# Kernel tuning notes

Hardware: AMD Instinct MI355X
Metric: run time of the kernel (lower is better)

Reference implementation:

```python
import jax, jax.numpy as jnp
import numpy as np

B, N, C, H = 4, 1024, 1024, 16
HD = C // H
SCALE = HD ** -0.5


def _init_linear(key, out_dim, in_dim):
    # torch nn.Linear default init: U(-1/sqrt(in), 1/sqrt(in)) for weight and bias
    kw, kb = jax.random.split(key)
    bound = 1.0 / np.sqrt(in_dim)
    W = jax.random.uniform(kw, (out_dim, in_dim), jnp.float32, -bound, bound)
    b = jax.random.uniform(kb, (out_dim,), jnp.float32, -bound, bound)
    return W, b


def setup_inputs() -> dict:
    key = jax.random.key(0)
    ks = jax.random.split(key, 5)
    x = jax.random.normal(ks[0], (B, N, C), jnp.float32)
    # NdLinear qkv: Linear(N->N) along seq axis, then Linear(C->3C) along channel axis
    Wq0, bq0 = _init_linear(ks[1], N, N)
    Wq1, bq1 = _init_linear(ks[2], 3 * C, C)
    # NdLinear proj: Linear(N->N) along seq axis, then Linear(C->C) along channel axis
    Wp0, bp0 = _init_linear(ks[3], N, N)
    Wp1, bp1 = _init_linear(ks[4], C, C)
    return {"x": x, "Wq0": Wq0, "bq0": bq0, "Wq1": Wq1, "bq1": bq1,
            "Wp0": Wp0, "bp0": bp0, "Wp1": Wp1, "bp1": bp1}


def _ndlinear(x, W0, b0, W1, b1):
    # NdLinear over (seq, channel): apply Linear along axis 1, then axis 2.
    # torch Linear: y = x @ W.T + b
    x = jnp.einsum('bnc,mn->bmc', x, W0) + b0[None, :, None]   # seq axis
    x = jnp.einsum('bnc,dc->bnd', x, W1) + b1                  # channel axis
    return x


def reference(x, Wq0, bq0, Wq1, bq1, Wp0, bp0, Wp1, bp1):
    qkv = _ndlinear(x, Wq0, bq0, Wq1, bq1)                     # (B, N, 3C)
    qkv = qkv.reshape(B, N, 3, H, HD).transpose(2, 0, 3, 1, 4) # (3, B, H, N, HD)
    q, k, v = qkv[0], qkv[1], qkv[2]
    attn = jnp.einsum('bhnd,bhmd->bhnm', q, k) * SCALE         # (B, H, N, N)
    attn = jax.nn.softmax(attn, axis=-1)
    out = jnp.einsum('bhnm,bhmd->bhnd', attn, v)               # (B, H, N, HD)
    out = out.transpose(0, 2, 1, 3).reshape(B, N, C)
    out = _ndlinear(out, Wp0, bp0, Wp1, bp1)
    return out
```

## Files before the change

### kernel.cpp

```cpp
#include <hip/hip_runtime.h>
#include <hip/hip_bf16.h>
#include <stdint.h>

typedef __bf16 bf16;
typedef __bf16 bf16x4 __attribute__((ext_vector_type(4)));
typedef __bf16 bf16x8 __attribute__((ext_vector_type(8)));
typedef float f32x4 __attribute__((ext_vector_type(4)));

#define B_ 4
#define N_ 1024
#define C_ 1024
#define H_ 16
#define MEG (1u << 20)

__device__ __forceinline__ uint32_t lds_off(const void* p) {
    return (uint32_t)(uintptr_t)p;
}
__device__ __forceinline__ void g2l16(const void* g, uint32_t lds_byte) {
    __builtin_amdgcn_global_load_lds(
        (const __attribute__((address_space(1))) unsigned int*)(uintptr_t)g,
        (__attribute__((address_space(3))) unsigned int*)(uintptr_t)lds_byte,
        16, 0, 0);
}

__global__ __launch_bounds__(256) void cvt4_k(
    const float* __restrict__ s0, bf16* __restrict__ d0,
    const float* __restrict__ s1, bf16* __restrict__ d1,
    const float* __restrict__ s2, bf16* __restrict__ d2,
    const float* __restrict__ s3, bf16* __restrict__ d3) {
    int bid = blockIdx.x;
    const float* s; bf16* d; int base;
    if (bid < 512)       { s = s0; d = d0; base = 0; }
    else if (bid < 2048) { s = s1; d = d1; base = 512; }
    else if (bid < 2560) { s = s2; d = d2; base = 2048; }
    else                 { s = s3; d = d3; base = 2560; }
    int i = ((bid - base) * 256 + threadIdx.x) * 8;
    float4 a = *(const float4*)(s + i);
    float4 b = *(const float4*)(s + i + 4);
    bf16x8 r;
    r[0] = (bf16)a.x; r[1] = (bf16)a.y; r[2] = (bf16)a.z; r[3] = (bf16)a.w;
    r[4] = (bf16)b.x; r[5] = (bf16)b.y; r[6] = (bf16)b.z; r[7] = (bf16)b.w;
    *(bf16x8*)(d + i) = r;
}

__global__ __launch_bounds__(256) void xpose_k(const float* __restrict__ x,
                                               bf16* __restrict__ xT) {
    __shared__ bf16 t[64][66];
    const int tid = threadIdx.x;
    const int b = blockIdx.z, n0 = blockIdx.y * 64, c0 = blockIdx.x * 64;
    {
        int nl = tid >> 2, seg = tid & 3;
        const float* src = x + ((size_t)b * N_ + n0 + nl) * C_ + c0 + seg * 16;
#pragma unroll
        for (int i = 0; i < 4; ++i) {
            float4 v = *(const float4*)(src + i * 4);
            t[nl][seg * 16 + i * 4 + 0] = (bf16)v.x;
            t[nl][seg * 16 + i * 4 + 1] = (bf16)v.y;
            t[nl][seg * 16 + i * 4 + 2] = (bf16)v.z;
            t[nl][seg * 16 + i * 4 + 3] = (bf16)v.w;
        }
    }
    __syncthreads();
    {
        int cl = tid >> 2, seg = tid & 3;
        bf16* dst = xT + ((size_t)b * C_ + c0 + cl) * N_ + n0 + seg * 16;
        bf16x8 o0, o1;
#pragma unroll
        for (int j = 0; j < 8; ++j) o0[j] = t[seg * 16 + j][cl];
#pragma unroll
        for (int j = 0; j < 8; ++j) o1[j] = t[seg * 16 + 8 + j][cl];
        *(bf16x8*)dst = o0;
        *(bf16x8*)(dst + 8) = o1;
    }
}

template <int BIAS, bool OF32>
__global__ __launch_bounds__(512) void gemm_k(
    const bf16* __restrict__ A, const bf16* __restrict__ Bm,
    const float* __restrict__ bias, void* __restrict__ Cv,
    int M, int Nn, int K, long long sA, long long sB, long long sC)
{
    __shared__ bf16 smem[2][2][128 * 64];

    const int tid = threadIdx.x;
    const int lane = tid & 63, wid = tid >> 6;
    const int lr = lane & 15, lg = lane >> 4;
    const int wr = wid >> 2, wc = wid & 3;
    const int m0 = blockIdx.y * 128, n0 = blockIdx.x * 128;

    const bf16* Ab = A + (size_t)blockIdx.z * sA;
    const bf16* Bb = Bm + (size_t)blockIdx.z * sB;

    const uint32_t a_lds0 = lds_off(&smem[0][0][0]);
    const uint32_t b_lds0 = lds_off(&smem[0][1][0]);
    const uint32_t bufstride = 2 * 128 * 64 * 2;

    auto stage = [&](int kt, int buf) {
#pragma unroll
        for (int half = 0; half < 2; ++half) {
            int it = tid + half * 512;
            int r = it >> 3, ch = it & 7;
            int sch = ch ^ (r & 7);
            g2l16(Ab + (size_t)(m0 + r) * K + kt * 64 + sch * 8,
                  a_lds0 + buf * bufstride + it * 16);
            g2l16(Bb + (size_t)(n0 + r) * K + kt * 64 + sch * 8,
                  b_lds0 + buf * bufstride + it * 16);
        }
    };

    f32x4 acc[4][2];
#pragma unroll
    for (int i = 0; i < 4; ++i)
#pragma unroll
        for (int j = 0; j < 2; ++j) { f32x4 z = {0.f,0.f,0.f,0.f}; acc[i][j] = z; }

    stage(0, 0);
    __syncthreads();

    const int nt = K >> 6;
    for (int t = 0; t < nt; ++t) {
        int buf = t & 1;
        if (t + 1 < nt) stage(t + 1, buf ^ 1);
        const bf16* As = &smem[buf][0][0];
        const bf16* Bs = &smem[buf][1][0];
#pragma unroll
        for (int s = 0; s < 2; ++s) {
            bf16x8 af[4], bfr[2];
#pragma unroll
            for (int mi = 0; mi < 4; ++mi) {
                int row = wr * 64 + mi * 16 + lr;
                int slot = (s * 4 + lg) ^ (row & 7);
                af[mi] = *(const bf16x8*)(As + row * 64 + slot * 8);
            }
#pragma unroll
            for (int ni = 0; ni < 2; ++ni) {
                int row = wc * 32 + ni * 16 + lr;
                int slot = (s * 4 + lg) ^ (row & 7);
                bfr[ni] = *(const bf16x8*)(Bs + row * 64 + slot * 8);
            }
#pragma unroll
            for (int mi = 0; mi < 4; ++mi)
#pragma unroll
                for (int ni = 0; ni < 2; ++ni)
                    acc[mi][ni] = __builtin_amdgcn_mfma_f32_16x16x32_bf16(
                        af[mi], bfr[ni], acc[mi][ni], 0, 0, 0);
        }
        __syncthreads();
    }

#pragma unroll
    for (int mi = 0; mi < 4; ++mi)
#pragma unroll
        for (int ni = 0; ni < 2; ++ni)
#pragma unroll
            for (int r = 0; r < 4; ++r) {
                int row = m0 + wr * 64 + mi * 16 + lg * 4 + r;
                int col = n0 + wc * 32 + ni * 16 + lr;
                float bv = (BIAS == 0) ? bias[row] : bias[col];
                float v = acc[mi][ni][r] + bv;
                if constexpr (OF32)
                    ((float*)Cv + (size_t)blockIdx.z * sC)[(size_t)row * Nn + col] = v;
                else
                    ((bf16*)Cv + (size_t)blockIdx.z * sC)[(size_t)row * Nn + col] = (bf16)v;
            }
}

__global__ __launch_bounds__(512) void attn_k(
    const bf16* __restrict__ qkv, bf16* __restrict__ aoT)
{
    __shared__ bf16 Ks[2][4096];
    __shared__ bf16 Vs[2][4096];
    __shared__ bf16 pbuf[8][1024];

    const int tid = threadIdx.x;
    const int lane = tid & 63, wid = tid >> 6;
    const int lr = lane & 15, lg = lane >> 4;
    const int bid = blockIdx.x;
    const int qt = bid >> 6, hb = bid & 63;
    const int b = hb >> 4, h = hb & 15;
    const int qrow0 = qt * 128 + wid * 16;
    const int hoff = h * 64;
    const bf16* qkvb = qkv + (size_t)b * (N_ * 3 * C_);

    bf16x8 qf[2];
#pragma unroll
    for (int kk = 0; kk < 2; ++kk) {
        qf[kk] = *(const bf16x8*)(qkvb + (size_t)(qrow0 + lr) * 3072 +
                                  hoff + kk * 32 + lg * 8);
#pragma unroll
        for (int j = 0; j < 8; ++j)
            qf[kk][j] = (bf16)((float)qf[kk][j] * 0.18033688f);
    }

    const uint32_t ks0 = lds_off(&Ks[0][0]);
    const int vd = tid & 63, vkg = tid >> 6;

    auto stageK = [&](int kt, int buf) {
        int key = tid >> 3, ch = tid & 7;
        int sch = ch ^ (key & 7);
        g2l16(qkvb + (size_t)(kt * 64 + key) * 3072 + C_ + hoff + sch * 8,
              ks0 + buf * 8192 + tid * 16);
    };
    auto loadV = [&](int kt) -> bf16x8 {
        const bf16* base = qkvb + 2 * C_ + hoff + vd;
        bf16x8 v;
#pragma unroll
        for (int j = 0; j < 8; ++j)
            v[j] = base[(size_t)(kt * 64 + vkg * 8 + j) * 3072];
        return v;
    };
    auto writeV = [&](bf16x8 v, int buf) {
        *(bf16x8*)(&Vs[buf][vd * 64 + ((vkg ^ (vd & 7)) * 8)]) = v;
    };

    float lsum = 0.f;
    f32x4 o[4];
#pragma unroll
    for (int i = 0; i < 4; ++i) { f32x4 z = {0.f,0.f,0.f,0.f}; o[i] = z; }

    char* prow = (char*)&pbuf[wid][0] + lr * 128;
    const int swz = (lr & 7) << 4;

    stageK(0, 0);
    writeV(loadV(0), 0);
    __syncthreads();

    for (int kt = 0; kt < 16; ++kt) {
        int buf = kt & 1;
        bf16x8 vnext;
        if (kt + 1 < 16) {
            stageK(kt + 1, buf ^ 1);
            vnext = loadV(kt + 1);
        }

        f32x4 s[4];
        __builtin_amdgcn_s_setprio(1);
#pragma unroll
        for (int st = 0; st < 4; ++st) {
            f32x4 z = {0.f, 0.f, 0.f, 0.f};
#pragma unroll
            for (int kk = 0; kk < 2; ++kk) {
                int row = st * 16 + lr;
                int slot = (kk * 4 + lg) ^ (row & 7);
                bf16x8 kf = *(const bf16x8*)(&Ks[buf][row * 64 + slot * 8]);
                z = __builtin_amdgcn_mfma_f32_16x16x32_bf16(kf, qf[kk], z, 0, 0, 0);
            }
            s[st] = z;
        }
        __builtin_amdgcn_s_setprio(0);

#pragma unroll
        for (int st = 0; st < 4; ++st) {
            bf16x4 w;
#pragma unroll
            for (int r = 0; r < 4; ++r) {
                float e = __builtin_amdgcn_exp2f(s[st][r]);
                w[r] = (bf16)e;
                lsum += e;
            }
            *(bf16x4*)(prow + ((st * 32 + lg * 8) ^ swz)) = w;
        }

        bf16x8 pf[2];
        pf[0] = *(const bf16x8*)(prow + ((lg * 16) ^ swz));
        pf[1] = *(const bf16x8*)(prow + ((64 + lg * 16) ^ swz));

        __builtin_amdgcn_s_setprio(1);
#pragma unroll
        for (int dt = 0; dt < 4; ++dt) {
            int row = dt * 16 + lr;
            bf16x8 v0 = *(const bf16x8*)(&Vs[buf][row * 64 + ((lg ^ (lr & 7)) * 8)]);
            bf16x8 v1 = *(const bf16x8*)(&Vs[buf][row * 64 + (((4 + lg) ^ (lr & 7)) * 8)]);
            o[dt] = __builtin_amdgcn_mfma_f32_16x16x32_bf16(pf[0], v0, o[dt], 0, 0, 0);
            o[dt] = __builtin_amdgcn_mfma_f32_16x16x32_bf16(pf[1], v1, o[dt], 0, 0, 0);
        }
        __builtin_amdgcn_s_setprio(0);

        if (kt + 1 < 16) writeV(vnext, buf ^ 1);
        __syncthreads();
    }

    lsum += __shfl_xor(lsum, 16, 64);
    lsum += __shfl_xor(lsum, 32, 64);
    float rtot = 1.0f / lsum;
    float rcpo[4];
#pragma unroll
    for (int r = 0; r < 4; ++r) rcpo[r] = __shfl(rtot, lg * 4 + r, 64);

#pragma unroll
    for (int dt = 0; dt < 4; ++dt) {
        bf16x4 ov;
#pragma unroll
        for (int r = 0; r < 4; ++r) ov[r] = (bf16)(o[dt][r] * rcpo[r]);
        size_t c = (size_t)b * C_ + hoff + dt * 16 + lr;
        *(bf16x4*)(aoT + c * N_ + qrow0 + lg * 4) = ov;
    }
}

extern "C" void kernel_launch(void* const* d_in, const int* in_sizes, int n_in,
                              void* d_out, int out_size, void* d_ws, size_t ws_size,
                              hipStream_t stream) {
    (void)in_sizes; (void)n_in; (void)out_size; (void)ws_size;
    const float* x   = (const float*)d_in[0];
    const float* Wq0 = (const float*)d_in[1];
    const float* bq0 = (const float*)d_in[2];
    const float* Wq1 = (const float*)d_in[3];
    const float* bq1 = (const float*)d_in[4];
    const float* Wp0 = (const float*)d_in[5];
    const float* bp0 = (const float*)d_in[6];
    const float* Wp1 = (const float*)d_in[7];
    const float* bp1 = (const float*)d_in[8];

    bf16* ws   = (bf16*)d_ws;
    bf16* xT   = ws;
    bf16* Wq0b = ws + 4 * MEG;
    bf16* Wq1b = ws + 5 * MEG;
    bf16* Wp0b = ws + 8 * MEG;
    bf16* Wp1b = ws + 9 * MEG;
    bf16* y1   = ws + 10 * MEG;
    bf16* y2   = ws + 14 * MEG;
    bf16* aoT  = y1;
    bf16* z1   = y2;
    float* outp = (float*)d_out;

    const long long s1M = (long long)N_ * C_;

    cvt4_k<<<dim3(3072), 256, 0, stream>>>(Wq0, Wq0b, Wq1, Wq1b,
                                           Wp0, Wp0b, Wp1, Wp1b);
    xpose_k<<<dim3(16, 16, 4), 256, 0, stream>>>(x, xT);

    gemm_k<0, false><<<dim3(8, 8, 4), 512, 0, stream>>>(
        Wq0b, xT, bq0, y1, 1024, 1024, 1024, 0LL, s1M, s1M);
    gemm_k<1, false><<<dim3(24, 32, 1), 512, 0, stream>>>(
        y1, Wq1b, bq1, y2, 4096, 3072, 1024, 0LL, 0LL, 0LL);
    attn_k<<<dim3(512), 512, 0, stream>>>(y2, aoT);
    gemm_k<0, false><<<dim3(8, 8, 4), 512, 0, stream>>>(
        Wp0b, aoT, bp0, z1, 1024, 1024, 1024, 0LL, s1M, s1M);
    gemm_k<1, true><<<dim3(8, 32, 1), 512, 0, stream>>>(
        z1, Wp1b, bp1, outp, 4096, 1024, 1024, 0LL, 0LL, 0LL);
}
```

Before: 121.1 us.

## Merge weight-convert and transpose kernels; split attention into 64-row query tiles

Folds the fp32-to-bf16 weight conversion and the x transpose into a single prep launch, saving one kernel launch. The attention kernel now uses 256 threads with 64 query rows per block and 1024 blocks instead of 512, to spread the work over more CUs on the MI355X. Each thread now stages two K chunks and two V chunks per tile, so K/V global traffic per query row doubles in exchange for more parallelism.

Measured after the change: 123.1 us. No clear change (+1.6%).

```diff
diff --git a/kernel.cpp b/kernel.cpp
--- a/kernel.cpp
+++ b/kernel.cpp
@@ -23,31 +23,33 @@
         16, 0, 0);
 }
 
-__global__ __launch_bounds__(256) void cvt4_k(
+__global__ __launch_bounds__(256) void prep_k(
+    const float* __restrict__ x, bf16* __restrict__ xT,
     const float* __restrict__ s0, bf16* __restrict__ d0,
     const float* __restrict__ s1, bf16* __restrict__ d1,
     const float* __restrict__ s2, bf16* __restrict__ d2,
-    const float* __restrict__ s3, bf16* __restrict__ d3) {
-    int bid = blockIdx.x;
-    const float* s; bf16* d; int base;
-    if (bid < 512)       { s = s0; d = d0; base = 0; }
-    else if (bid < 2048) { s = s1; d = d1; base = 512; }
-    else if (bid < 2560) { s = s2; d = d2; base = 2048; }
-    else                 { s = s3; d = d3; base = 2560; }
-    int i = ((bid - base) * 256 + threadIdx.x) * 8;
-    float4 a = *(const float4*)(s + i);
-    float4 b = *(const float4*)(s + i + 4);
-    bf16x8 r;
-    r[0] = (bf16)a.x; r[1] = (bf16)a.y; r[2] = (bf16)a.z; r[3] = (bf16)a.w;
-    r[4] = (bf16)b.x; r[5] = (bf16)b.y; r[6] = (bf16)b.z; r[7] = (bf16)b.w;
-    *(bf16x8*)(d + i) = r;
-}
-
-__global__ __launch_bounds__(256) void xpose_k(const float* __restrict__ x,
-                                               bf16* __restrict__ xT) {
+    const float* __restrict__ s3, bf16* __restrict__ d3)
+{
     __shared__ bf16 t[64][66];
+    const int bid = blockIdx.x;
     const int tid = threadIdx.x;
-    const int b = blockIdx.z, n0 = blockIdx.y * 64, c0 = blockIdx.x * 64;
+    if (bid < 3072) {
+        const float* s; bf16* d; int base;
+        if (bid < 512)       { s = s0; d = d0; base = 0; }
+        else if (bid < 2048) { s = s1; d = d1; base = 512; }
+        else if (bid < 2560) { s = s2; d = d2; base = 2048; }
+        else                 { s = s3; d = d3; base = 2560; }
+        int i = ((bid - base) * 256 + tid) * 8;
+        float4 a = *(const float4*)(s + i);
+        float4 b = *(const float4*)(s + i + 4);
+        bf16x8 r;
+        r[0] = (bf16)a.x; r[1] = (bf16)a.y; r[2] = (bf16)a.z; r[3] = (bf16)a.w;
+        r[4] = (bf16)b.x; r[5] = (bf16)b.y; r[6] = (bf16)b.z; r[7] = (bf16)b.w;
+        *(bf16x8*)(d + i) = r;
+        return;
+    }
+    const int idx = bid - 3072;
+    const int c0 = (idx & 15) * 64, n0 = ((idx >> 4) & 15) * 64, b = idx >> 8;
     {
         int nl = tid >> 2, seg = tid & 3;
         const float* src = x + ((size_t)b * N_ + n0 + nl) * C_ + c0 + seg * 16;
@@ -165,12 +167,12 @@
             }
 }
 
-__global__ __launch_bounds__(512) void attn_k(
+__global__ __launch_bounds__(256) void attn_k(
     const bf16* __restrict__ qkv, bf16* __restrict__ aoT)
 {
     __shared__ bf16 Ks[2][4096];
     __shared__ bf16 Vs[2][4096];
-    __shared__ bf16 pbuf[8][1024];
+    __shared__ bf16 pbuf[4][1024];
 
     const int tid = threadIdx.x;
     const int lane = tid & 63, wid = tid >> 6;
@@ -178,7 +180,7 @@
     const int bid = blockIdx.x;
     const int qt = bid >> 6, hb = bid & 63;
     const int b = hb >> 4, h = hb & 15;
-    const int qrow0 = qt * 128 + wid * 16;
+    const int qrow0 = qt * 64 + wid * 16;
     const int hoff = h * 64;
     const bf16* qkvb = qkv + (size_t)b * (N_ * 3 * C_);
 
@@ -196,21 +198,31 @@
     const int vd = tid & 63, vkg = tid >> 6;
 
     auto stageK = [&](int kt, int buf) {
-        int key = tid >> 3, ch = tid & 7;
-        int sch = ch ^ (key & 7);
-        g2l16(qkvb + (size_t)(kt * 64 + key) * 3072 + C_ + hoff + sch * 8,
-              ks0 + buf * 8192 + tid * 16);
+#pragma unroll
+        for (int hh = 0; hh < 2; ++hh) {
+            int it = tid + hh * 256;
+            int key = it >> 3, ch = it & 7;
+            int sch = ch ^ (key & 7);
+            g2l16(qkvb + (size_t)(kt * 64 + key) * 3072 + C_ + hoff + sch * 8,
+                  ks0 + buf * 8192 + it * 16);
+        }
     };
-    auto loadV = [&](int kt) -> bf16x8 {
+    auto loadV = [&](int kt, bf16x8 v[2]) {
         const bf16* base = qkvb + 2 * C_ + hoff + vd;
-        bf16x8 v;
-#pragma unroll
-        for (int j = 0; j < 8; ++j)
-            v[j] = base[(size_t)(kt * 64 + vkg * 8 + j) * 3072];
-        return v;
+#pragma unroll
+        for (int hh = 0; hh < 2; ++hh) {
+            int kg = vkg + hh * 4;
+#pragma unroll
+            for (int j = 0; j < 8; ++j)
+                v[hh][j] = base[(size_t)(kt * 64 + kg * 8 + j) * 3072];
+        }
     };
-    auto writeV = [&](bf16x8 v, int buf) {
-        *(bf16x8*)(&Vs[buf][vd * 64 + ((vkg ^ (vd & 7)) * 8)]) = v;
+    auto writeV = [&](bf16x8 v[2], int buf) {
+#pragma unroll
+        for (int hh = 0; hh < 2; ++hh) {
+            int kg = vkg + hh * 4;
+            *(bf16x8*)(&Vs[buf][vd * 64 + ((kg ^ (vd & 7)) * 8)]) = v[hh];
+        }
     };
 
     float lsum = 0.f;
@@ -221,16 +233,18 @@
     char* prow = (char*)&pbuf[wid][0] + lr * 128;
     const int swz = (lr & 7) << 4;
 
+    bf16x8 v0buf[2];
     stageK(0, 0);
-    writeV(loadV(0), 0);
+    loadV(0, v0buf);
+    writeV(v0buf, 0);
     __syncthreads();
 
     for (int kt = 0; kt < 16; ++kt) {
         int buf = kt & 1;
-        bf16x8 vnext;
+        bf16x8 vnext[2];
         if (kt + 1 < 16) {
             stageK(kt + 1, buf ^ 1);
-            vnext = loadV(kt + 1);
+            loadV(kt + 1, vnext);
         }
 
         f32x4 s[4];
@@ -325,15 +339,14 @@
 
     const long long s1M = (long long)N_ * C_;
 
-    cvt4_k<<<dim3(3072), 256, 0, stream>>>(Wq0, Wq0b, Wq1, Wq1b,
+    prep_k<<<dim3(4096), 256, 0, stream>>>(x, xT, Wq0, Wq0b, Wq1, Wq1b,
                                            Wp0, Wp0b, Wp1, Wp1b);
-    xpose_k<<<dim3(16, 16, 4), 256, 0, stream>>>(x, xT);
 
     gemm_k<0, false><<<dim3(8, 8, 4), 512, 0, stream>>>(
         Wq0b, xT, bq0, y1, 1024, 1024, 1024, 0LL, s1M, s1M);
     gemm_k<1, false><<<dim3(24, 32, 1), 512, 0, stream>>>(
         y1, Wq1b, bq1, y2, 4096, 3072, 1024, 0LL, 0LL, 0LL);
-    attn_k<<<dim3(512), 512, 0, stream>>>(y2, aoT);
+    attn_k<<<dim3(1024), 256, 0, stream>>>(y2, aoT);
     gemm_k<0, false><<<dim3(8, 8, 4), 512, 0, stream>>>(
         Wp0b, aoT, bp0, z1, 1024, 1024, 1024, 0LL, s1M, s1M);
     gemm_k<1, true><<<dim3(8, 32, 1), 512, 0, stream>>>(
```
